# Performance work log

Hardware: AMD Instinct MI355X
Metric: run time of the kernel (lower is better)

The kernel has to match this reference:

```python
import jax, jax.numpy as jnp
import numpy as np

D = 1024      # model_dim
DK = 1024     # keys_dim
DV = 1024     # values_dim
H = 16        # heads
HDK = DK // H # per-head key dim (64)
HDV = DV // H
FF = 2048     # FFN default hidden_dim
EPS = 1e-5


def setup_inputs() -> dict:
    key = jax.random.key(0)
    ks = jax.random.split(key, 16)
    s = lambda k, sh, fan: jax.random.normal(k, sh, jnp.float32) * (1.0 / np.sqrt(fan))
    return {
        "x": jax.random.normal(ks[0], (8, 1024, D), jnp.float32),
        # per-head projections stored as [D, H, hd] (concat of the H small Linears)
        "Wq": s(ks[1], (D, H, HDK), D), "bq": jnp.zeros((H, HDK), jnp.float32),
        "Wk": s(ks[2], (D, H, HDK), D), "bk": jnp.zeros((H, HDK), jnp.float32),
        "Wv": s(ks[3], (D, H, HDV), D), "bv": jnp.zeros((H, HDV), jnp.float32),
        "Wo": s(ks[4], (DV, D), DV), "bo": jnp.zeros((D,), jnp.float32),
        "ln1_g": jnp.ones((D,), jnp.float32), "ln1_b": jnp.zeros((D,), jnp.float32),
        "W1": s(ks[5], (D, FF), D), "b1": jnp.zeros((FF,), jnp.float32),
        "W2": s(ks[6], (FF, D), FF), "b2": jnp.zeros((D,), jnp.float32),
        "ln2_g": jnp.ones((D,), jnp.float32), "ln2_b": jnp.zeros((D,), jnp.float32),
    }


def layer_norm(x, g, b):
    mu = jnp.mean(x, axis=-1, keepdims=True)
    var = jnp.mean(jnp.square(x - mu), axis=-1, keepdims=True)
    return (x - mu) * jax.lax.rsqrt(var + EPS) * g + b


def reference(x, Wq, bq, Wk, bk, Wv, bv, Wo, bo, ln1_g, ln1_b, W1, b1, W2, b2, ln2_g, ln2_b):
    # per-head projections (equivalent to H small Linears, batched)
    q = jnp.einsum("bsd,dhk->bhsk", x, Wq) + bq[:, None, :]
    k = jnp.einsum("bsd,dhk->bhsk", x, Wk) + bk[:, None, :]
    v = jnp.einsum("bsd,dhv->bhsv", x, Wv) + bv[:, None, :]
    # scaled dot-product attention per head (scale uses per-head dk)
    scores = jnp.einsum("bhsk,bhtk->bhst", q, k) / jnp.sqrt(jnp.float32(HDK))
    w = jax.nn.softmax(scores, axis=-1)
    ctx = jnp.einsum("bhst,bhtv->bhsv", w, v)           # [B,H,S,hdv]
    B, _, S, _ = ctx.shape
    ctx = ctx.transpose(0, 2, 1, 3).reshape(B, S, DV)   # concat heads
    c = ctx @ Wo + bo
    h = layer_norm(x + c, ln1_g, ln1_b)
    y = jax.nn.relu(h @ W1 + b1) @ W2 + b2
    return layer_norm(h + y, ln2_g, ln2_b)
```

## Files before the change

### kernel.cpp

```cpp
#include <hip/hip_runtime.h>
#include <hip/hip_bf16.h>
#include <cstdint>

typedef __bf16 bf16_t;
typedef __bf16 bf16x8 __attribute__((ext_vector_type(8)));
typedef __bf16 bf16x4 __attribute__((ext_vector_type(4)));
typedef float f32x4 __attribute__((ext_vector_type(4)));

#define SEQ    1024
#define BATCH  8
#define NTOK   8192
#define DMODEL 1024
#define NHEAD  16
#define HD     64
#define FFDIM  2048

__device__ __forceinline__ void async16(const void* g, void* l) {
  __builtin_amdgcn_global_load_lds(
      (const __attribute__((address_space(1))) void*)g,
      (__attribute__((address_space(3))) void*)l, 16, 0, 0);
}

__global__ __launch_bounds__(256)
void cast_bf16_kernel(const float* __restrict__ in, bf16_t* __restrict__ out, int n4) {
  int i = blockIdx.x * 256 + threadIdx.x;
  if (i >= n4) return;
  float4 v = ((const float4*)in)[i];
  bf16x4 o = { (bf16_t)v.x, (bf16_t)v.y, (bf16_t)v.z, (bf16_t)v.w };
  *(bf16x4*)&out[(size_t)i * 4] = o;
}

__global__ __launch_bounds__(256)
void transpose_cast_kernel(const float* __restrict__ W, bf16_t* __restrict__ Wt,
                           int R, int C) {
  __shared__ float tile[32][33];
  const int bx = blockIdx.x * 32;
  const int by = blockIdx.y * 32;
  const int tx = threadIdx.x;
  const int ty = threadIdx.y;
#pragma unroll
  for (int i = 0; i < 4; ++i)
    tile[ty + 8 * i][tx] = W[(size_t)(by + ty + 8 * i) * C + bx + tx];
  __syncthreads();
#pragma unroll
  for (int i = 0; i < 4; ++i)
    Wt[(size_t)(bx + ty + 8 * i) * R + by + tx] = (bf16_t)tile[tx][ty + 8 * i];
}

template <int EPI>
__global__ __launch_bounds__(256)
void gemm_bt(const bf16_t* __restrict__ A, const bf16_t* __restrict__ Bt,
             const float* __restrict__ bias, void* __restrict__ outp,
             int M, int N, int K, float scale) {
  __shared__ bf16_t As[128 * 64];
  __shared__ bf16_t Bs[128 * 64];
  const int tid = threadIdx.x;
  const int wave = tid >> 6, lane = tid & 63;
  const int wr = (wave >> 1) * 64, wc = (wave & 1) * 64;
  const int bm = blockIdx.x * 128, bn = blockIdx.y * 128;

  f32x4 acc[4][4];
#pragma unroll
  for (int i = 0; i < 4; ++i)
#pragma unroll
    for (int j = 0; j < 4; ++j) acc[i][j] = (f32x4){0.f, 0.f, 0.f, 0.f};

  const int lcol = (lane & 7) * 8;
  const int fr = lane & 15, kg = (lane >> 4) * 8;

  const int nk = K >> 6;
  for (int kt = 0; kt < nk; ++kt) {
    const int k0 = kt << 6;
#pragma unroll
    for (int i = 0; i < 4; ++i) {
      const int chunk = i * 4 + wave;
      const int row = chunk * 8 + (lane >> 3);
      async16(&A[(size_t)(bm + row) * K + k0 + lcol], &As[chunk * 512]);
      async16(&Bt[(size_t)(bn + row) * K + k0 + lcol], &Bs[chunk * 512]);
    }
    asm volatile("s_waitcnt vmcnt(0)" ::: "memory");
    __syncthreads();

#pragma unroll
    for (int kk = 0; kk < 2; ++kk) {
      bf16x8 a[4], b[4];
      const int ko = kk * 32 + kg;
#pragma unroll
      for (int i = 0; i < 4; ++i) a[i] = *(const bf16x8*)&As[(wr + i * 16 + fr) * 64 + ko];
#pragma unroll
      for (int j = 0; j < 4; ++j) b[j] = *(const bf16x8*)&Bs[(wc + j * 16 + fr) * 64 + ko];
#pragma unroll
      for (int i = 0; i < 4; ++i)
#pragma unroll
        for (int j = 0; j < 4; ++j)
          acc[i][j] = __builtin_amdgcn_mfma_f32_16x16x32_bf16(a[i], b[j], acc[i][j], 0, 0, 0);
    }
    __syncthreads();
  }

  const int lr = (lane >> 4) * 4, lc = lane & 15;
#pragma unroll
  for (int j = 0; j < 4; ++j) {
    const int col = bn + wc + j * 16 + lc;
    const float bv = bias[col];
#pragma unroll
    for (int i = 0; i < 4; ++i) {
#pragma unroll
      for (int r = 0; r < 4; ++r) {
        const int row = bm + wr + i * 16 + lr + r;
        const float v = (acc[i][j][r] + bv) * scale;
        if (EPI == 0) {
          ((float*)outp)[(size_t)row * N + col] = v;
        } else if (EPI == 1) {
          ((bf16_t*)outp)[(size_t)row * N + col] = (bf16_t)fmaxf(v, 0.f);
        } else if (EPI == 2) {
          const int b_ = row >> 10, s_ = row & 1023, h_ = col >> 6, e_ = col & 63;
          ((bf16_t*)outp)[((size_t)((b_ * NHEAD + h_) * SEQ + s_)) * HD + e_] = (bf16_t)v;
        } else {
          const int b_ = row >> 10, s_ = row & 1023, h_ = col >> 6, e_ = col & 63;
          ((bf16_t*)outp)[((size_t)((b_ * NHEAD + h_) * HD + e_)) * SEQ + s_] = (bf16_t)v;
        }
      }
    }
  }
}

__global__ __launch_bounds__(256)
void attn_kernel(const bf16_t* __restrict__ Q, const bf16_t* __restrict__ K,
                 const bf16_t* __restrict__ VT, bf16_t* __restrict__ CTX) {
  const int bh = blockIdx.x;
  const int qt = blockIdx.y * 128;
  const int b_ = bh >> 4, h_ = bh & 15;
  const bf16_t* qh = Q + (size_t)bh * SEQ * HD;
  const bf16_t* kh = K + (size_t)bh * SEQ * HD;
  const bf16_t* vh = VT + (size_t)bh * HD * SEQ;
  const int tid = threadIdx.x, wave = tid >> 6, lane = tid & 63;
  const int fr = lane & 15, kg = (lane >> 4) * 8;
  const int lr = (lane >> 4) * 4, lc = lane & 15;

  __shared__ bf16_t Ks[2][64 * 64];
  __shared__ bf16_t Vs[2][64 * 64];
  __shared__ bf16_t Ps[128 * 64];

  const int srow = lane >> 3;
  const int scol = ((lane & 7) ^ srow) * 8;

  bf16x8 qf[2][2];
#pragma unroll
  for (int i = 0; i < 2; ++i)
#pragma unroll
    for (int kk = 0; kk < 2; ++kk)
      qf[i][kk] = *(const bf16x8*)&qh[(size_t)(qt + wave * 32 + i * 16 + fr) * HD + kk * 32 + kg];

  f32x4 octx[2][4];
  float mrun[2][4], lrun[2][4];
#pragma unroll
  for (int i = 0; i < 2; ++i)
#pragma unroll
    for (int j = 0; j < 4; ++j) octx[i][j] = (f32x4){0.f, 0.f, 0.f, 0.f};
#pragma unroll
  for (int i = 0; i < 2; ++i)
#pragma unroll
    for (int r = 0; r < 4; ++r) { mrun[i][r] = -1e30f; lrun[i][r] = 0.f; }

  auto stage = [&](int buf, int t) {
#pragma unroll
    for (int i = 0; i < 2; ++i) {
      const int ch = i * 4 + wave;
      const int row = ch * 8 + srow;
      async16(&kh[(size_t)(t * 64 + row) * HD + scol], &Ks[buf][ch * 512]);
      async16(&vh[(size_t)row * SEQ + t * 64 + scol], &Vs[buf][ch * 512]);
    }
  };

  stage(0, 0);
  asm volatile("s_waitcnt vmcnt(0)" ::: "memory");
  __syncthreads();

  for (int t = 0; t < SEQ / 64; ++t) {
    const int cur = t & 1;
    if (t + 1 < SEQ / 64) stage(cur ^ 1, t + 1);

    f32x4 sc[2][4];
#pragma unroll
    for (int i = 0; i < 2; ++i)
#pragma unroll
      for (int j = 0; j < 4; ++j) sc[i][j] = (f32x4){0.f, 0.f, 0.f, 0.f};
#pragma unroll
    for (int kk = 0; kk < 2; ++kk) {
      bf16x8 kf[4];
#pragma unroll
      for (int j = 0; j < 4; ++j) {
        const int row = j * 16 + fr;
        kf[j] = *(const bf16x8*)&Ks[cur][row * 64 + ((kk * 32 + kg) ^ ((row & 7) << 3))];
      }
#pragma unroll
      for (int i = 0; i < 2; ++i)
#pragma unroll
        for (int j = 0; j < 4; ++j)
          sc[i][j] = __builtin_amdgcn_mfma_f32_16x16x32_bf16(qf[i][kk], kf[j], sc[i][j], 0, 0, 0);
    }

    float pmx[2][4];
    int ok = 1;
#pragma unroll
    for (int i = 0; i < 2; ++i)
#pragma unroll
      for (int r = 0; r < 4; ++r) {
        const float m3 = fmaxf(fmaxf(sc[i][0][r], sc[i][1][r]),
                               fmaxf(sc[i][2][r], sc[i][3][r]));
        pmx[i][r] = m3;
        ok &= (m3 <= mrun[i][r] + 8.f) ? 1 : 0;
      }
    if (!__all(ok)) {
#pragma unroll
      for (int i = 0; i < 2; ++i)
#pragma unroll
        for (int r = 0; r < 4; ++r) {
          float mx = pmx[i][r];
#pragma unroll
          for (int m = 1; m < 16; m <<= 1) mx = fmaxf(mx, __shfl_xor(mx, m));
          const float mnew = fmaxf(mrun[i][r], mx);
          const float alpha = exp2f(mrun[i][r] - mnew);
          mrun[i][r] = mnew;
          lrun[i][r] *= alpha;
#pragma unroll
          for (int j = 0; j < 4; ++j) octx[i][j][r] *= alpha;
        }
    }
#pragma unroll
    for (int i = 0; i < 2; ++i)
#pragma unroll
      for (int r = 0; r < 4; ++r) {
        const float m = mrun[i][r];
        float s = 0.f;
#pragma unroll
        for (int j = 0; j < 4; ++j) {
          const float p = exp2f(sc[i][j][r] - m);
          sc[i][j][r] = p;
          s += p;
        }
        lrun[i][r] += s;
        const int prow = wave * 32 + i * 16 + lr + r;
#pragma unroll
        for (int j = 0; j < 4; ++j)
          Ps[prow * 64 + (((j * 16 + lc)) ^ ((prow & 7) << 3))] = (bf16_t)sc[i][j][r];
      }
    asm volatile("s_waitcnt lgkmcnt(0)" ::: "memory");

#pragma unroll
    for (int kk = 0; kk < 2; ++kk) {
      bf16x8 pf[2], vf[4];
#pragma unroll
      for (int i = 0; i < 2; ++i) {
        const int row = wave * 32 + i * 16 + fr;
        pf[i] = *(const bf16x8*)&Ps[row * 64 + ((kk * 32 + kg) ^ ((row & 7) << 3))];
      }
#pragma unroll
      for (int j = 0; j < 4; ++j) {
        const int row = j * 16 + fr;
        vf[j] = *(const bf16x8*)&Vs[cur][row * 64 + ((kk * 32 + kg) ^ ((row & 7) << 3))];
      }
#pragma unroll
      for (int i = 0; i < 2; ++i)
#pragma unroll
        for (int j = 0; j < 4; ++j)
          octx[i][j] = __builtin_amdgcn_mfma_f32_16x16x32_bf16(pf[i], vf[j], octx[i][j], 0, 0, 0);
    }

    asm volatile("s_waitcnt vmcnt(0)" ::: "memory");
    __syncthreads();
  }

#pragma unroll
  for (int i = 0; i < 2; ++i)
#pragma unroll
    for (int r = 0; r < 4; ++r) {
      float l = lrun[i][r];
#pragma unroll
      for (int m = 1; m < 16; m <<= 1) l += __shfl_xor(l, m);
      const float inv = 1.f / l;
      const int row = qt + wave * 32 + i * 16 + lr + r;
#pragma unroll
      for (int j = 0; j < 4; ++j) {
        const int c = j * 16 + lc;
        CTX[((size_t)(b_ * SEQ + row)) * DMODEL + h_ * HD + c] = (bf16_t)(octx[i][j][r] * inv);
      }
    }
}

__global__ __launch_bounds__(256)
void ln_kernel(const float* __restrict__ X, const float* __restrict__ Y,
               const float* __restrict__ g, const float* __restrict__ b,
               float* __restrict__ outf, bf16_t* __restrict__ outb) {
  const int row = blockIdx.x, tid = threadIdx.x;
  const int wave = tid >> 6, lane = tid & 63;
  const float4 xv = ((const float4*)X)[(size_t)row * 256 + tid];
  const float4 yv = ((const float4*)Y)[(size_t)row * 256 + tid];
  const float s0 = xv.x + yv.x, s1 = xv.y + yv.y, s2 = xv.z + yv.z, s3 = xv.w + yv.w;
  float sum = s0 + s1 + s2 + s3;
  float sq = s0 * s0 + s1 * s1 + s2 * s2 + s3 * s3;
#pragma unroll
  for (int off = 1; off < 64; off <<= 1) {
    sum += __shfl_xor(sum, off);
    sq += __shfl_xor(sq, off);
  }
  __shared__ float red[8];
  if (lane == 0) { red[wave] = sum; red[4 + wave] = sq; }
  __syncthreads();
  sum = red[0] + red[1] + red[2] + red[3];
  sq = red[4] + red[5] + red[6] + red[7];
  const float mu = sum * (1.f / 1024.f);
  const float var = sq * (1.f / 1024.f) - mu * mu;
  const float rstd = rsqrtf(var + 1e-5f);
  const float4 gv = ((const float4*)g)[tid];
  const float4 bv = ((const float4*)b)[tid];
  const float o0 = (s0 - mu) * rstd * gv.x + bv.x;
  const float o1 = (s1 - mu) * rstd * gv.y + bv.y;
  const float o2 = (s2 - mu) * rstd * gv.z + bv.z;
  const float o3 = (s3 - mu) * rstd * gv.w + bv.w;
  ((float4*)outf)[(size_t)row * 256 + tid] = make_float4(o0, o1, o2, o3);
  if (outb) {
    bf16x4 ob = { (bf16_t)o0, (bf16_t)o1, (bf16_t)o2, (bf16_t)o3 };
    *(bf16x4*)&outb[(size_t)row * 1024 + tid * 4] = ob;
  }
}

extern "C" void kernel_launch(void* const* d_in, const int* in_sizes, int n_in,
                              void* d_out, int out_size, void* d_ws, size_t ws_size,
                              hipStream_t stream) {
  const float* x   = (const float*)d_in[0];
  const float* Wq  = (const float*)d_in[1];
  const float* bq  = (const float*)d_in[2];
  const float* Wk  = (const float*)d_in[3];
  const float* bk  = (const float*)d_in[4];
  const float* Wv  = (const float*)d_in[5];
  const float* bv  = (const float*)d_in[6];
  const float* Wo  = (const float*)d_in[7];
  const float* bo  = (const float*)d_in[8];
  const float* g1  = (const float*)d_in[9];
  const float* be1 = (const float*)d_in[10];
  const float* W1  = (const float*)d_in[11];
  const float* b1  = (const float*)d_in[12];
  const float* W2  = (const float*)d_in[13];
  const float* b2  = (const float*)d_in[14];
  const float* g2  = (const float*)d_in[15];
  const float* be2 = (const float*)d_in[16];

  char* ws = (char*)d_ws;
  size_t off = 0;
  auto alloc = [&](size_t bytes) {
    char* p = ws + off;
    off += (bytes + 255) & ~(size_t)255;
    return p;
  };
  const size_t MB = 1u << 20;
  bf16_t* xb  = (bf16_t*)alloc(16 * MB);
  bf16_t* WqT = (bf16_t*)alloc(2 * MB);
  bf16_t* WkT = (bf16_t*)alloc(2 * MB);
  bf16_t* WvT = (bf16_t*)alloc(2 * MB);
  bf16_t* WoT = (bf16_t*)alloc(2 * MB);
  bf16_t* W1T = (bf16_t*)alloc(4 * MB);
  bf16_t* W2T = (bf16_t*)alloc(4 * MB);
  bf16_t* qb  = (bf16_t*)alloc(16 * MB);
  bf16_t* kb  = (bf16_t*)alloc(16 * MB);
  bf16_t* vT  = (bf16_t*)alloc(16 * MB);
  float*  attnf = (float*)alloc(32 * MB);
  float*  h     = (float*)alloc(32 * MB);
  bf16_t* ctx = xb;
  bf16_t* hb  = qb;
  bf16_t* u   = kb;
  float*  y   = attnf;

  cast_bf16_kernel<<<dim3(NTOK * DMODEL / 4 / 256), dim3(256), 0, stream>>>(x, xb, NTOK * DMODEL / 4);
  transpose_cast_kernel<<<dim3(32, 32), dim3(32, 8), 0, stream>>>(Wq, WqT, 1024, 1024);
  transpose_cast_kernel<<<dim3(32, 32), dim3(32, 8), 0, stream>>>(Wk, WkT, 1024, 1024);
  transpose_cast_kernel<<<dim3(32, 32), dim3(32, 8), 0, stream>>>(Wv, WvT, 1024, 1024);
  transpose_cast_kernel<<<dim3(32, 32), dim3(32, 8), 0, stream>>>(Wo, WoT, 1024, 1024);
  transpose_cast_kernel<<<dim3(64, 32), dim3(32, 8), 0, stream>>>(W1, W1T, 1024, 2048);
  transpose_cast_kernel<<<dim3(32, 64), dim3(32, 8), 0, stream>>>(W2, W2T, 2048, 1024);

  const float qscale = 0.125f * 1.44269504088896f;
  gemm_bt<2><<<dim3(64, 8), dim3(256), 0, stream>>>(xb, WqT, bq, qb, NTOK, DMODEL, DMODEL, qscale);
  gemm_bt<2><<<dim3(64, 8), dim3(256), 0, stream>>>(xb, WkT, bk, kb, NTOK, DMODEL, DMODEL, 1.0f);
  gemm_bt<3><<<dim3(64, 8), dim3(256), 0, stream>>>(xb, WvT, bv, vT, NTOK, DMODEL, DMODEL, 1.0f);

  attn_kernel<<<dim3(128, 8), dim3(256), 0, stream>>>(qb, kb, vT, ctx);

  gemm_bt<0><<<dim3(64, 8), dim3(256), 0, stream>>>(ctx, WoT, bo, attnf, NTOK, DMODEL, DMODEL, 1.0f);
  ln_kernel<<<dim3(NTOK), dim3(256), 0, stream>>>(x, attnf, g1, be1, h, hb);

  gemm_bt<1><<<dim3(64, 16), dim3(256), 0, stream>>>(hb, W1T, b1, u, NTOK, FFDIM, DMODEL, 1.0f);
  gemm_bt<0><<<dim3(64, 8), dim3(256), 0, stream>>>(u, W2T, b2, y, NTOK, DMODEL, FFDIM, 1.0f);
  ln_kernel<<<dim3(NTOK), dim3(256), 0, stream>>>(h, y, g2, be2, (float*)d_out, nullptr);
}
```

Measured before the change: 370.6 us.

## Replace GEMMs with pipelined 256x256 kernel, fuse QKV, split-K FFN2

Replaces the 128x128 single-buffered GEMM with a 512-thread 256x256-tile kernel. It double-buffers LDS and stores operands in a fragment-ready layout. Asynchronous loads of each half-tile are interleaved with quarter-tile MFMA phases, using barriers and raised wave priority around the math. The three Q/K/V projections become one launch over a concatenated weight, with per-column-range epilogues. The FFN down-projection uses split-K into two fp32 partial buffers that LayerNorm2 sums. LayerNorm1 now writes only a bf16 output, and that bf16 copy is reused as the residual, which saves traffic but lowers the residual's precision. The Wo GEMM launches only 128 workgroups, which may leave compute units idle.

```diff
diff --git a/kernel.cpp b/kernel.cpp
--- a/kernel.cpp
+++ b/kernel.cpp
@@ -20,6 +20,8 @@
       (const __attribute__((address_space(1))) void*)g,
       (__attribute__((address_space(3))) void*)l, 16, 0, 0);
 }
+
+#define BARRIER() do { __builtin_amdgcn_s_barrier(); asm volatile("" ::: "memory"); } while (0)
 
 __global__ __launch_bounds__(256)
 void cast_bf16_kernel(const float* __restrict__ in, bf16_t* __restrict__ out, int n4) {
@@ -48,81 +50,192 @@
 }
 
 template <int EPI>
-__global__ __launch_bounds__(256)
-void gemm_bt(const bf16_t* __restrict__ A, const bf16_t* __restrict__ Bt,
-             const float* __restrict__ bias, void* __restrict__ outp,
-             int M, int N, int K, float scale) {
-  __shared__ bf16_t As[128 * 64];
-  __shared__ bf16_t Bs[128 * 64];
+__global__ __launch_bounds__(512)
+void gemm256(const bf16_t* __restrict__ A, int lda,
+             const bf16_t* __restrict__ Bt, int ldb,
+             int K, int nTN, int nInner, int kOffA, int kOffB, size_t outStride,
+             const float* __restrict__ bias0, const float* __restrict__ bias1,
+             const float* __restrict__ bias2,
+             void* __restrict__ o0, void* __restrict__ o1, void* __restrict__ o2,
+             int ldo, float qscale) {
+  __shared__ bf16_t As[2][16384];
+  __shared__ bf16_t Bs[2][16384];
   const int tid = threadIdx.x;
-  const int wave = tid >> 6, lane = tid & 63;
-  const int wr = (wave >> 1) * 64, wc = (wave & 1) * 64;
-  const int bm = blockIdx.x * 128, bn = blockIdx.y * 128;
-
-  f32x4 acc[4][4];
-#pragma unroll
-  for (int i = 0; i < 4; ++i)
+  const int w = tid >> 6, l = tid & 63;
+  const int fr = l & 15, ks = l >> 4;
+
+  const int nwg = gridDim.x, bid = blockIdx.x;
+  int wg = (bid & 7) * (nwg >> 3) + (bid >> 3);
+  const int kz = wg / nInner; wg -= kz * nInner;
+  const int tm = wg / nTN, tn = wg - tm * nTN;
+  const int bm = tm << 8, bn = tn << 8;
+  A  += (size_t)kz * kOffA;
+  Bt += (size_t)kz * kOffB;
+
+  const int wm = w >> 2, wn = w & 3;
+
+  size_t aoff[2], boff[2];
+  int ldsSub[2];
+#pragma unroll
+  for (int j = 0; j < 2; ++j) {
+    const int sub = 8 * j + w, rtil = sub >> 1, ctil = sub & 1;
+    aoff[j] = (size_t)(rtil * 16 + fr) * lda + ctil * 32 + ks * 8;
+    boff[j] = (size_t)(rtil * 16 + fr) * ldb + ctil * 32 + ks * 8;
+    ldsSub[j] = sub * 512;
+  }
+
+  f32x4 acc[8][4];
+#pragma unroll
+  for (int i = 0; i < 8; ++i)
 #pragma unroll
     for (int j = 0; j < 4; ++j) acc[i][j] = (f32x4){0.f, 0.f, 0.f, 0.f};
 
-  const int lcol = (lane & 7) * 8;
-  const int fr = lane & 15, kg = (lane >> 4) * 8;
-
   const int nk = K >> 6;
-  for (int kt = 0; kt < nk; ++kt) {
-    const int k0 = kt << 6;
-#pragma unroll
-    for (int i = 0; i < 4; ++i) {
-      const int chunk = i * 4 + wave;
-      const int row = chunk * 8 + (lane >> 3);
-      async16(&A[(size_t)(bm + row) * K + k0 + lcol], &As[chunk * 512]);
-      async16(&Bt[(size_t)(bn + row) * K + k0 + lcol], &Bs[chunk * 512]);
+  const int totHT = nk << 2;
+  int g = 0;
+
+  auto issue_ht = [&](int gg) {
+    const int tau = gg >> 2, ht = gg & 3;
+    const int slot = tau & 1, h = ht >> 1;
+    if (ht == 0 || ht == 3) {
+#pragma unroll
+      for (int j = 0; j < 2; ++j)
+        async16(A + (size_t)(bm + h * 128) * lda + (size_t)tau * 64 + aoff[j],
+                &As[slot][h * 8192 + ldsSub[j]]);
+    } else {
+#pragma unroll
+      for (int j = 0; j < 2; ++j)
+        async16(Bt + (size_t)(bn + h * 128) * ldb + (size_t)tau * 64 + boff[j],
+                &Bs[slot][h * 8192 + ldsSub[j]]);
     }
-    asm volatile("s_waitcnt vmcnt(0)" ::: "memory");
-    __syncthreads();
-
-#pragma unroll
-    for (int kk = 0; kk < 2; ++kk) {
-      bf16x8 a[4], b[4];
-      const int ko = kk * 32 + kg;
-#pragma unroll
-      for (int i = 0; i < 4; ++i) a[i] = *(const bf16x8*)&As[(wr + i * 16 + fr) * 64 + ko];
-#pragma unroll
-      for (int j = 0; j < 4; ++j) b[j] = *(const bf16x8*)&Bs[(wc + j * 16 + fr) * 64 + ko];
-#pragma unroll
-      for (int i = 0; i < 4; ++i)
-#pragma unroll
-        for (int j = 0; j < 4; ++j)
-          acc[i][j] = __builtin_amdgcn_mfma_f32_16x16x32_bf16(a[i], b[j], acc[i][j], 0, 0, 0);
-    }
-    __syncthreads();
+  };
+
+  for (; g < 4; ++g) issue_ht(g);
+  asm volatile("s_waitcnt vmcnt(4)" ::: "memory");
+  BARRIER();
+
+  bf16x8 afr[4][2], b0fr[2][2], b1fr[2][2];
+
+  for (int tc = 0; tc < nk; ++tc) {
+    const bool lastT = (tc == nk - 1);
+    const bf16_t* Asl = As[tc & 1];
+    const bf16_t* Bsl = Bs[tc & 1];
+
+#pragma unroll
+    for (int m = 0; m < 4; ++m)
+#pragma unroll
+      for (int kk = 0; kk < 2; ++kk)
+        afr[m][kk] = *(const bf16x8*)&Asl[((wm * 4 + m) * 2 + kk) * 512 + l * 8];
+#pragma unroll
+    for (int n = 0; n < 2; ++n)
+#pragma unroll
+      for (int kk = 0; kk < 2; ++kk)
+        b0fr[n][kk] = *(const bf16x8*)&Bsl[((wn * 2 + n) * 2 + kk) * 512 + l * 8];
+    if (g < totHT) { issue_ht(g); ++g; }
+    if (lastT) asm volatile("s_waitcnt vmcnt(2)" ::: "memory");
+    else       asm volatile("s_waitcnt vmcnt(4)" ::: "memory");
+    BARRIER();
+    __builtin_amdgcn_s_setprio(1);
+#pragma unroll
+    for (int m = 0; m < 4; ++m)
+#pragma unroll
+      for (int n = 0; n < 2; ++n)
+#pragma unroll
+        for (int kk = 0; kk < 2; ++kk)
+          acc[m][n] = __builtin_amdgcn_mfma_f32_16x16x32_bf16(afr[m][kk], b0fr[n][kk], acc[m][n], 0, 0, 0);
+    __builtin_amdgcn_s_setprio(0);
+    BARRIER();
+
+#pragma unroll
+    for (int n = 0; n < 2; ++n)
+#pragma unroll
+      for (int kk = 0; kk < 2; ++kk)
+        b1fr[n][kk] = *(const bf16x8*)&Bsl[8192 + ((wn * 2 + n) * 2 + kk) * 512 + l * 8];
+    if (g < totHT) { issue_ht(g); ++g; }
+    if (lastT) asm volatile("s_waitcnt vmcnt(0)" ::: "memory");
+    else       asm volatile("s_waitcnt vmcnt(4)" ::: "memory");
+    BARRIER();
+    __builtin_amdgcn_s_setprio(1);
+#pragma unroll
+    for (int m = 0; m < 4; ++m)
+#pragma unroll
+      for (int n = 0; n < 2; ++n)
+#pragma unroll
+        for (int kk = 0; kk < 2; ++kk)
+          acc[m][2 + n] = __builtin_amdgcn_mfma_f32_16x16x32_bf16(afr[m][kk], b1fr[n][kk], acc[m][2 + n], 0, 0, 0);
+    __builtin_amdgcn_s_setprio(0);
+    BARRIER();
+
+#pragma unroll
+    for (int m = 0; m < 4; ++m)
+#pragma unroll
+      for (int kk = 0; kk < 2; ++kk)
+        afr[m][kk] = *(const bf16x8*)&Asl[8192 + ((wm * 4 + m) * 2 + kk) * 512 + l * 8];
+    if (g < totHT) { issue_ht(g); ++g; }
+    BARRIER();
+    __builtin_amdgcn_s_setprio(1);
+#pragma unroll
+    for (int m = 0; m < 4; ++m)
+#pragma unroll
+      for (int n = 0; n < 2; ++n)
+#pragma unroll
+        for (int kk = 0; kk < 2; ++kk)
+          acc[4 + m][2 + n] = __builtin_amdgcn_mfma_f32_16x16x32_bf16(afr[m][kk], b1fr[n][kk], acc[4 + m][2 + n], 0, 0, 0);
+    __builtin_amdgcn_s_setprio(0);
+    BARRIER();
+
+    if (g < totHT) { issue_ht(g); ++g; }
+    if (!lastT) asm volatile("s_waitcnt vmcnt(4)" ::: "memory");
+    BARRIER();
+    __builtin_amdgcn_s_setprio(1);
+#pragma unroll
+    for (int m = 0; m < 4; ++m)
+#pragma unroll
+      for (int n = 0; n < 2; ++n)
+#pragma unroll
+        for (int kk = 0; kk < 2; ++kk)
+          acc[4 + m][n] = __builtin_amdgcn_mfma_f32_16x16x32_bf16(afr[m][kk], b0fr[n][kk], acc[4 + m][n], 0, 0, 0);
+    __builtin_amdgcn_s_setprio(0);
+    BARRIER();
   }
 
-  const int lr = (lane >> 4) * 4, lc = lane & 15;
-#pragma unroll
-  for (int j = 0; j < 4; ++j) {
-    const int col = bn + wc + j * 16 + lc;
-    const float bv = bias[col];
-#pragma unroll
-    for (int i = 0; i < 4; ++i) {
-#pragma unroll
-      for (int r = 0; r < 4; ++r) {
-        const int row = bm + wr + i * 16 + lr + r;
-        const float v = (acc[i][j][r] + bv) * scale;
-        if (EPI == 0) {
-          ((float*)outp)[(size_t)row * N + col] = v;
-        } else if (EPI == 1) {
-          ((bf16_t*)outp)[(size_t)row * N + col] = (bf16_t)fmaxf(v, 0.f);
-        } else if (EPI == 2) {
-          const int b_ = row >> 10, s_ = row & 1023, h_ = col >> 6, e_ = col & 63;
-          ((bf16_t*)outp)[((size_t)((b_ * NHEAD + h_) * SEQ + s_)) * HD + e_] = (bf16_t)v;
-        } else {
-          const int b_ = row >> 10, s_ = row & 1023, h_ = col >> 6, e_ = col & 63;
-          ((bf16_t*)outp)[((size_t)((b_ * NHEAD + h_) * HD + e_)) * SEQ + s_] = (bf16_t)v;
+  const int mode = bn >> 10;
+#pragma unroll
+  for (int q = 0; q < 2; ++q)
+#pragma unroll
+    for (int m = 0; m < 4; ++m)
+#pragma unroll
+      for (int pq = 0; pq < 2; ++pq)
+#pragma unroll
+        for (int n = 0; n < 2; ++n) {
+          const int mi = q * 4 + m, nj = pq * 2 + n;
+          const int col = bn + pq * 128 + wn * 32 + n * 16 + fr;
+          const int rowb = bm + q * 128 + wm * 64 + m * 16 + ks * 4;
+#pragma unroll
+          for (int r = 0; r < 4; ++r) {
+            const int row = rowb + r;
+            const float v = acc[mi][nj][r];
+            if (EPI == 0) {
+              const float bv = (kz == 0 && bias0) ? bias0[col] : 0.f;
+              ((float*)o0)[kz * outStride + (size_t)row * ldo + col] = v + bv;
+            } else if (EPI == 1) {
+              ((bf16_t*)o0)[(size_t)row * ldo + col] = (bf16_t)fmaxf(v + bias0[col], 0.f);
+            } else {
+              const int cl = col & 1023;
+              const int b_ = row >> 10, s_ = row & 1023, h_ = cl >> 6, e_ = cl & 63;
+              if (mode == 0) {
+                ((bf16_t*)o0)[((size_t)((b_ * NHEAD + h_) * SEQ + s_)) * HD + e_] =
+                    (bf16_t)((v + bias0[cl]) * qscale);
+              } else if (mode == 1) {
+                ((bf16_t*)o1)[((size_t)((b_ * NHEAD + h_) * SEQ + s_)) * HD + e_] =
+                    (bf16_t)(v + bias1[cl]);
+              } else {
+                ((bf16_t*)o2)[((size_t)((b_ * NHEAD + h_) * HD + e_)) * SEQ + s_] =
+                    (bf16_t)(v + bias2[cl]);
+              }
+            }
+          }
         }
-      }
-    }
-  }
 }
 
 __global__ __launch_bounds__(256)
@@ -276,10 +389,10 @@
   for (int i = 0; i < 2; ++i)
 #pragma unroll
     for (int r = 0; r < 4; ++r) {
-      float l = lrun[i][r];
-#pragma unroll
-      for (int m = 1; m < 16; m <<= 1) l += __shfl_xor(l, m);
-      const float inv = 1.f / l;
+      float lsum = lrun[i][r];
+#pragma unroll
+      for (int m = 1; m < 16; m <<= 1) lsum += __shfl_xor(lsum, m);
+      const float inv = 1.f / lsum;
       const int row = qt + wave * 32 + i * 16 + lr + r;
 #pragma unroll
       for (int j = 0; j < 4; ++j) {
@@ -290,13 +403,13 @@
 }
 
 __global__ __launch_bounds__(256)
-void ln_kernel(const float* __restrict__ X, const float* __restrict__ Y,
-               const float* __restrict__ g, const float* __restrict__ b,
-               float* __restrict__ outf, bf16_t* __restrict__ outb) {
+void ln1_kernel(const float* __restrict__ X, const float* __restrict__ Y0,
+                const float* __restrict__ g, const float* __restrict__ b,
+                bf16_t* __restrict__ outb) {
   const int row = blockIdx.x, tid = threadIdx.x;
   const int wave = tid >> 6, lane = tid & 63;
   const float4 xv = ((const float4*)X)[(size_t)row * 256 + tid];
-  const float4 yv = ((const float4*)Y)[(size_t)row * 256 + tid];
+  const float4 yv = ((const float4*)Y0)[(size_t)row * 256 + tid];
   const float s0 = xv.x + yv.x, s1 = xv.y + yv.y, s2 = xv.z + yv.z, s3 = xv.w + yv.w;
   float sum = s0 + s1 + s2 + s3;
   float sq = s0 * s0 + s1 * s1 + s2 * s2 + s3 * s3;
@@ -315,15 +428,44 @@
   const float rstd = rsqrtf(var + 1e-5f);
   const float4 gv = ((const float4*)g)[tid];
   const float4 bv = ((const float4*)b)[tid];
-  const float o0 = (s0 - mu) * rstd * gv.x + bv.x;
-  const float o1 = (s1 - mu) * rstd * gv.y + bv.y;
-  const float o2 = (s2 - mu) * rstd * gv.z + bv.z;
-  const float o3 = (s3 - mu) * rstd * gv.w + bv.w;
-  ((float4*)outf)[(size_t)row * 256 + tid] = make_float4(o0, o1, o2, o3);
-  if (outb) {
-    bf16x4 ob = { (bf16_t)o0, (bf16_t)o1, (bf16_t)o2, (bf16_t)o3 };
-    *(bf16x4*)&outb[(size_t)row * 1024 + tid * 4] = ob;
+  bf16x4 ob = { (bf16_t)((s0 - mu) * rstd * gv.x + bv.x),
+                (bf16_t)((s1 - mu) * rstd * gv.y + bv.y),
+                (bf16_t)((s2 - mu) * rstd * gv.z + bv.z),
+                (bf16_t)((s3 - mu) * rstd * gv.w + bv.w) };
+  *(bf16x4*)&outb[(size_t)row * 1024 + tid * 4] = ob;
+}
+
+__global__ __launch_bounds__(256)
+void ln2_kernel(const bf16_t* __restrict__ Hb, const float* __restrict__ Y0,
+                const float* __restrict__ Y1, const float* __restrict__ g,
+                const float* __restrict__ b, float* __restrict__ outf) {
+  const int row = blockIdx.x, tid = threadIdx.x;
+  const int wave = tid >> 6, lane = tid & 63;
+  const bf16x4 hv = *(const bf16x4*)&Hb[(size_t)row * 1024 + tid * 4];
+  const float4 y0 = ((const float4*)Y0)[(size_t)row * 256 + tid];
+  const float4 y1 = ((const float4*)Y1)[(size_t)row * 256 + tid];
+  const float s0 = (float)hv[0] + y0.x + y1.x, s1 = (float)hv[1] + y0.y + y1.y;
+  const float s2 = (float)hv[2] + y0.z + y1.z, s3 = (float)hv[3] + y0.w + y1.w;
+  float sum = s0 + s1 + s2 + s3;
+  float sq = s0 * s0 + s1 * s1 + s2 * s2 + s3 * s3;
+#pragma unroll
+  for (int off = 1; off < 64; off <<= 1) {
+    sum += __shfl_xor(sum, off);
+    sq += __shfl_xor(sq, off);
   }
+  __shared__ float red[8];
+  if (lane == 0) { red[wave] = sum; red[4 + wave] = sq; }
+  __syncthreads();
+  sum = red[0] + red[1] + red[2] + red[3];
+  sq = red[4] + red[5] + red[6] + red[7];
+  const float mu = sum * (1.f / 1024.f);
+  const float var = sq * (1.f / 1024.f) - mu * mu;
+  const float rstd = rsqrtf(var + 1e-5f);
+  const float4 gv = ((const float4*)g)[tid];
+  const float4 bv = ((const float4*)b)[tid];
+  ((float4*)outf)[(size_t)row * 256 + tid] =
+      make_float4((s0 - mu) * rstd * gv.x + bv.x, (s1 - mu) * rstd * gv.y + bv.y,
+                  (s2 - mu) * rstd * gv.z + bv.z, (s3 - mu) * rstd * gv.w + bv.w);
 }
 
 extern "C" void kernel_launch(void* const* d_in, const int* in_sizes, int n_in,
@@ -348,49 +490,50 @@
   const float* be2 = (const float*)d_in[16];
 
   char* ws = (char*)d_ws;
-  size_t off = 0;
-  auto alloc = [&](size_t bytes) {
-    char* p = ws + off;
-    off += (bytes + 255) & ~(size_t)255;
-    return p;
-  };
   const size_t MB = 1u << 20;
-  bf16_t* xb  = (bf16_t*)alloc(16 * MB);
-  bf16_t* WqT = (bf16_t*)alloc(2 * MB);
-  bf16_t* WkT = (bf16_t*)alloc(2 * MB);
-  bf16_t* WvT = (bf16_t*)alloc(2 * MB);
-  bf16_t* WoT = (bf16_t*)alloc(2 * MB);
-  bf16_t* W1T = (bf16_t*)alloc(4 * MB);
-  bf16_t* W2T = (bf16_t*)alloc(4 * MB);
-  bf16_t* qb  = (bf16_t*)alloc(16 * MB);
-  bf16_t* kb  = (bf16_t*)alloc(16 * MB);
-  bf16_t* vT  = (bf16_t*)alloc(16 * MB);
-  float*  attnf = (float*)alloc(32 * MB);
-  float*  h     = (float*)alloc(32 * MB);
+  bf16_t* xb    = (bf16_t*)(ws + 0 * MB);
+  bf16_t* WqkvT = (bf16_t*)(ws + 16 * MB);
+  bf16_t* WoT   = (bf16_t*)(ws + 22 * MB);
+  bf16_t* W1T   = (bf16_t*)(ws + 24 * MB);
+  bf16_t* W2T   = (bf16_t*)(ws + 28 * MB);
+  bf16_t* qb    = (bf16_t*)(ws + 32 * MB);
+  bf16_t* kb    = (bf16_t*)(ws + 48 * MB);
+  bf16_t* vT    = (bf16_t*)(ws + 64 * MB);
+  float*  y0    = (float*)(ws + 80 * MB);
+  float*  y1    = (float*)(ws + 112 * MB);
   bf16_t* ctx = xb;
   bf16_t* hb  = qb;
   bf16_t* u   = kb;
-  float*  y   = attnf;
 
   cast_bf16_kernel<<<dim3(NTOK * DMODEL / 4 / 256), dim3(256), 0, stream>>>(x, xb, NTOK * DMODEL / 4);
-  transpose_cast_kernel<<<dim3(32, 32), dim3(32, 8), 0, stream>>>(Wq, WqT, 1024, 1024);
-  transpose_cast_kernel<<<dim3(32, 32), dim3(32, 8), 0, stream>>>(Wk, WkT, 1024, 1024);
-  transpose_cast_kernel<<<dim3(32, 32), dim3(32, 8), 0, stream>>>(Wv, WvT, 1024, 1024);
+  transpose_cast_kernel<<<dim3(32, 32), dim3(32, 8), 0, stream>>>(Wq, WqkvT, 1024, 1024);
+  transpose_cast_kernel<<<dim3(32, 32), dim3(32, 8), 0, stream>>>(Wk, WqkvT + 1024 * 1024, 1024, 1024);
+  transpose_cast_kernel<<<dim3(32, 32), dim3(32, 8), 0, stream>>>(Wv, WqkvT + 2 * 1024 * 1024, 1024, 1024);
   transpose_cast_kernel<<<dim3(32, 32), dim3(32, 8), 0, stream>>>(Wo, WoT, 1024, 1024);
   transpose_cast_kernel<<<dim3(64, 32), dim3(32, 8), 0, stream>>>(W1, W1T, 1024, 2048);
   transpose_cast_kernel<<<dim3(32, 64), dim3(32, 8), 0, stream>>>(W2, W2T, 2048, 1024);
 
   const float qscale = 0.125f * 1.44269504088896f;
-  gemm_bt<2><<<dim3(64, 8), dim3(256), 0, stream>>>(xb, WqT, bq, qb, NTOK, DMODEL, DMODEL, qscale);
-  gemm_bt<2><<<dim3(64, 8), dim3(256), 0, stream>>>(xb, WkT, bk, kb, NTOK, DMODEL, DMODEL, 1.0f);
-  gemm_bt<3><<<dim3(64, 8), dim3(256), 0, stream>>>(xb, WvT, bv, vT, NTOK, DMODEL, DMODEL, 1.0f);
+
+  gemm256<2><<<dim3(384), dim3(512), 0, stream>>>(
+      xb, 1024, WqkvT, 1024, 1024, 12, 384, 0, 0, 0,
+      bq, bk, bv, qb, kb, vT, 0, qscale);
 
   attn_kernel<<<dim3(128, 8), dim3(256), 0, stream>>>(qb, kb, vT, ctx);
 
-  gemm_bt<0><<<dim3(64, 8), dim3(256), 0, stream>>>(ctx, WoT, bo, attnf, NTOK, DMODEL, DMODEL, 1.0f);
-  ln_kernel<<<dim3(NTOK), dim3(256), 0, stream>>>(x, attnf, g1, be1, h, hb);
-
-  gemm_bt<1><<<dim3(64, 16), dim3(256), 0, stream>>>(hb, W1T, b1, u, NTOK, FFDIM, DMODEL, 1.0f);
-  gemm_bt<0><<<dim3(64, 8), dim3(256), 0, stream>>>(u, W2T, b2, y, NTOK, DMODEL, FFDIM, 1.0f);
-  ln_kernel<<<dim3(NTOK), dim3(256), 0, stream>>>(h, y, g2, be2, (float*)d_out, nullptr);
-}
+  gemm256<0><<<dim3(128), dim3(512), 0, stream>>>(
+      ctx, 1024, WoT, 1024, 1024, 4, 128, 0, 0, 0,
+      bo, nullptr, nullptr, y0, nullptr, nullptr, 1024, 1.f);
+
+  ln1_kernel<<<dim3(NTOK), dim3(256), 0, stream>>>(x, y0, g1, be1, hb);
+
+  gemm256<1><<<dim3(256), dim3(512), 0, stream>>>(
+      hb, 1024, W1T, 1024, 1024, 8, 256, 0, 0, 0,
+      b1, nullptr, nullptr, u, nullptr, nullptr, 2048, 1.f);
+
+  gemm256<0><<<dim3(256), dim3(512), 0, stream>>>(
+      u, 2048, W2T, 2048, 1024, 4, 128, 1024, 1024, (size_t)NTOK * 1024,
+      b2, nullptr, nullptr, y0, nullptr, nullptr, 1024, 1.f);
+
+  ln2_kernel<<<dim3(NTOK), dim3(256), 0, stream>>>(hb, y0, y1, g2, be2, (float*)d_out);
+}
```

After: 440.0 us. +18.7%, slower.
